# Kernel optimization log

Measured on AMD Instinct MI355X. Metric: run time of the kernel, lower is better.

The kernel has to match this reference:

```python
import jax, jax.numpy as jnp
import numpy as np

DIM = 1024
DEPTH = 8
DIM_HEAD = 64
HEADS = 16
NUM_Q = 16
EMB = 768
OUT = 1024
FF_INNER = 4 * DIM
INNER = DIM_HEAD * HEADS  # 1024
B, N1 = 64, 577
EPS = 1e-5


def _ln(x, g, b):
    mu = jnp.mean(x, axis=-1, keepdims=True)
    var = jnp.mean((x - mu) ** 2, axis=-1, keepdims=True)
    return (x - mu) * jax.lax.rsqrt(var + EPS) * g + b


def setup_inputs() -> dict:
    key = jax.random.key(0)
    ks = jax.random.split(key, 16)
    std = 0.02
    inp = {
        'x': jax.random.normal(ks[0], (B, N1, EMB), jnp.float32),
        'queries': jax.random.normal(ks[1], (1, NUM_Q, DIM), jnp.float32) / DIM ** 0.5,
        'proj_in_w': jax.random.normal(ks[2], (EMB, DIM), jnp.float32) * std,
        'proj_in_b': jnp.zeros((DIM,), jnp.float32),
        'ln1_g': jnp.ones((DEPTH, DIM), jnp.float32),
        'ln1_b': jnp.zeros((DEPTH, DIM), jnp.float32),
        'ln2_g': jnp.ones((DEPTH, DIM), jnp.float32),
        'ln2_b': jnp.zeros((DEPTH, DIM), jnp.float32),
        'wq': jax.random.normal(ks[3], (DEPTH, DIM, INNER), jnp.float32) * std,
        'wkv': jax.random.normal(ks[4], (DEPTH, DIM, 2 * INNER), jnp.float32) * std,
        'wo': jax.random.normal(ks[5], (DEPTH, INNER, DIM), jnp.float32) * std,
        'ffln_g': jnp.ones((DEPTH, DIM), jnp.float32),
        'ffln_b': jnp.zeros((DEPTH, DIM), jnp.float32),
        'w1': jax.random.normal(ks[6], (DEPTH, DIM, FF_INNER), jnp.float32) * std,
        'w2': jax.random.normal(ks[7], (DEPTH, FF_INNER, DIM), jnp.float32) * std,
        'proj_out_w': jax.random.normal(ks[8], (DIM, OUT), jnp.float32) * std,
        'proj_out_b': jnp.zeros((OUT,), jnp.float32),
        'nout_g': jnp.ones((OUT,), jnp.float32),
        'nout_b': jnp.zeros((OUT,), jnp.float32),
    }
    return inp


def reference(x, queries, proj_in_w, proj_in_b, ln1_g, ln1_b, ln2_g, ln2_b,
              wq, wkv, wo, ffln_g, ffln_b, w1, w2,
              proj_out_w, proj_out_b, nout_g, nout_b):
    b = x.shape[0]
    xp = x @ proj_in_w + proj_in_b          # (b, n1, dim)
    latents0 = jnp.broadcast_to(queries, (b, NUM_Q, DIM))
    scale = DIM_HEAD ** -0.25               # applied to both q and k

    def layer(latents, p):
        (g1, b1, g2, b2, Wq, Wkv, Wo, gf, bf, W1, W2) = p
        xn = _ln(xp, g1, b1)                # (b, n1, dim)
        lt = _ln(latents, g2, b2)           # (b, nq, dim)
        q = lt @ Wq                         # (b, nq, inner)
        kv_in = jnp.concatenate([xn, lt], axis=1)   # (b, n1+nq, dim)
        kv = kv_in @ Wkv                    # (b, n1+nq, 2*inner)
        k, v = jnp.split(kv, 2, axis=-1)
        L = kv_in.shape[1]
        qh = q.reshape(b, NUM_Q, HEADS, DIM_HEAD).transpose(0, 2, 1, 3)
        kh = k.reshape(b, L, HEADS, DIM_HEAD).transpose(0, 2, 1, 3)
        vh = v.reshape(b, L, HEADS, DIM_HEAD).transpose(0, 2, 1, 3)
        logits = jnp.einsum('bhqd,bhkd->bhqk', qh * scale, kh * scale)
        w = jax.nn.softmax(logits.astype(jnp.float32), axis=-1).astype(logits.dtype)
        o = jnp.einsum('bhqk,bhkd->bhqd', w, vh)
        o = o.transpose(0, 2, 1, 3).reshape(b, NUM_Q, INNER) @ Wo
        latents = o + latents
        h = _ln(latents, gf, bf) @ W1
        h = jax.nn.gelu(h, approximate=False)
        latents = h @ W2 + latents
        return latents, None

    params = (ln1_g, ln1_b, ln2_g, ln2_b, wq, wkv, wo, ffln_g, ffln_b, w1, w2)
    latents, _ = jax.lax.scan(layer, latents0, params)
    out = latents @ proj_out_w + proj_out_b
    return _ln(out, nout_g, nout_b)
```

## Files before the change

### kernel.cpp

```cpp
#include <hip/hip_runtime.h>
#include <hip/hip_bf16.h>
#include <math.h>

#define DEV __device__ __forceinline__

typedef __bf16 bf16x8 __attribute__((ext_vector_type(8)));
typedef float f32x4 __attribute__((ext_vector_type(4)));
typedef unsigned short u16x8 __attribute__((ext_vector_type(8)));
typedef unsigned short u16x4 __attribute__((ext_vector_type(4)));

DEV float b2f(unsigned short u){ unsigned int i = ((unsigned int)u)<<16; float f; __builtin_memcpy(&f,&i,4); return f; }
DEV unsigned short f2b(float x){ unsigned int i; __builtin_memcpy(&i,&x,4); unsigned int r = i + 0x7FFFu + ((i>>16)&1u); return (unsigned short)(r>>16); }

DEV int swz(int row, int elem){ return row*64 + ((((elem>>3) ^ row) & 7)<<3) + (elem&7); }

DEV int xcd_swz(int orig, int nwg){
  int q = nwg >> 3, r = nwg & 7;
  int x = orig & 7, idx = orig >> 3;
  return (x < r ? x*(q+1) : r*(q+1) + (x-r)*q) + idx;
}

enum { EPI_F32=0, EPI_GELU=2, EPI_RESF32=3 };

__global__ __launch_bounds__(512)
void gemm3(const unsigned short* __restrict__ A, const unsigned short* __restrict__ Bt,
           const float* __restrict__ bias, unsigned short* __restrict__ Out,
           int M, int N, int K, int NT)
{
    __shared__ unsigned short As[256*64];
    __shared__ unsigned short Bs[256*64];
    const int tid  = threadIdx.x;
    const int lane = tid & 63;
    const int wave = tid >> 6;
    const int wr = wave >> 2, wc = wave & 3;
    const int nb = xcd_swz(blockIdx.x, gridDim.x);
    const int nt = nb % NT, mt = nb / NT;

    f32x4 acc[8][4];
    #pragma unroll
    for (int m=0;m<8;m++)
      #pragma unroll
      for (int n=0;n<4;n++) acc[m][n] = f32x4{0.f,0.f,0.f,0.f};

    const unsigned short* pA[4]; const unsigned short* pB[4];
    int dA[4], dB[4];
    #pragma unroll
    for (int i=0;i<4;i++){
      int e = (i*512+tid)*8; int row = e>>6, col = e&63;
      int gr = mt*256 + row; if (gr > M-1) gr = M-1;
      pA[i] = A + (size_t)gr*K + col;
      dA[i] = swz(row,col);
      pB[i] = Bt + (size_t)(nt*256+row)*K + col;
      dB[i] = swz(row,col);
    }

    u16x8 rA[4], rB[4];
    auto issue = [&](int k0){
      #pragma unroll
      for (int i=0;i<4;i++) rA[i] = *reinterpret_cast<const u16x8*>(pA[i]+k0);
      #pragma unroll
      for (int i=0;i<4;i++) rB[i] = *reinterpret_cast<const u16x8*>(pB[i]+k0);
    };
    auto commit = [&](){
      #pragma unroll
      for (int i=0;i<4;i++) *reinterpret_cast<u16x8*>(&As[dA[i]]) = rA[i];
      #pragma unroll
      for (int i=0;i<4;i++) *reinterpret_cast<u16x8*>(&Bs[dB[i]]) = rB[i];
    };

    issue(0);
    const int nk = K / 64;
    #pragma unroll 1
    for (int kt=0; kt<nk; kt++){
      __syncthreads();
      commit();
      __syncthreads();
      if (kt+1 < nk) issue((kt+1)*64);
      #pragma unroll
      for (int kk=0; kk<2; kk++){
        bf16x8 bv[4];
        #pragma unroll
        for (int n=0;n<4;n++){
          int r = wc*64 + n*16 + (lane&15);
          bv[n] = (bf16x8)(*reinterpret_cast<const u16x8*>(&Bs[swz(r, kk*32 + (lane>>4)*8)]));
        }
        #pragma unroll
        for (int m=0;m<8;m++){
          int r = wr*128 + m*16 + (lane&15);
          bf16x8 av = (bf16x8)(*reinterpret_cast<const u16x8*>(&As[swz(r, kk*32 + (lane>>4)*8)]));
          #pragma unroll
          for (int n=0;n<4;n++)
            acc[m][n] = __builtin_amdgcn_mfma_f32_16x16x32_bf16(av, bv[n], acc[m][n], 0, 0, 0);
        }
      }
    }

    #pragma unroll
    for (int m=0;m<8;m++){
      #pragma unroll
      for (int n=0;n<4;n++){
        #pragma unroll
        for (int r=0;r<4;r++){
          int row = mt*256 + wr*128 + m*16 + (lane>>4)*4 + r;
          int col = nt*256 + wc*64 + n*16 + (lane&15);
          if (row < M){
            float v = acc[m][n][r];
            if (bias) v += bias[col];
            Out[(size_t)row*N + col] = f2b(v);
          }
        }
      }
    }
}

template<int EPI>
__global__ __launch_bounds__(256)
void gemm_sp2(const unsigned short* __restrict__ AH, const unsigned short* __restrict__ AL,
              const unsigned short* __restrict__ BH, const unsigned short* __restrict__ BL,
              const float* __restrict__ bias, const float* __restrict__ Res,
              void* __restrict__ Out, unsigned short* __restrict__ OutL,
              int M, int N, int K, int NT)
{
    constexpr int MR=2, NR=2;
    __shared__ unsigned short As[2*64*64];
    __shared__ unsigned short Bs[2*64*64];
    const int tid  = threadIdx.x;
    const int lane = tid & 63;
    const int wave = tid >> 6;
    const int wr = wave >> 1, wc = wave & 1;
    const int chunk = gridDim.x >> 3;
    const int nb = (blockIdx.x & 7)*chunk + (blockIdx.x >> 3);
    const int nt = nb % NT, mt = nb / NT;

    f32x4 acc[MR][NR];
    #pragma unroll
    for (int m=0;m<MR;m++)
      #pragma unroll
      for (int n=0;n<NR;n++) acc[m][n] = f32x4{0.f,0.f,0.f,0.f};

    const unsigned short *pA[2], *pB[2];
    int dst[2];
    #pragma unroll
    for (int i=0;i<2;i++){
      int e = (i*256+tid)*8; int row = e>>6, col = e&63;
      pA[i] = AH + (size_t)(mt*64+row)*K + col;
      pB[i] = BH + (size_t)(nt*64+row)*K + col;
      dst[i] = swz(row,col);
    }
    const size_t dAL = (size_t)(AL - AH);
    const size_t dBL = (size_t)(BL - BH);

    u16x8 rAH0[2], rAL0[2], rBH0[2], rBL0[2];
    u16x8 rAH1[2], rAL1[2], rBH1[2], rBL1[2];
    auto issue0 = [&](int k0){
      #pragma unroll
      for (int i=0;i<2;i++){
        rAH0[i] = *reinterpret_cast<const u16x8*>(pA[i]+k0);
        rAL0[i] = *reinterpret_cast<const u16x8*>(pA[i]+dAL+k0);
        rBH0[i] = *reinterpret_cast<const u16x8*>(pB[i]+k0);
        rBL0[i] = *reinterpret_cast<const u16x8*>(pB[i]+dBL+k0);
      }
    };
    auto issue1 = [&](int k0){
      #pragma unroll
      for (int i=0;i<2;i++){
        rAH1[i] = *reinterpret_cast<const u16x8*>(pA[i]+k0);
        rAL1[i] = *reinterpret_cast<const u16x8*>(pA[i]+dAL+k0);
        rBH1[i] = *reinterpret_cast<const u16x8*>(pB[i]+k0);
        rBL1[i] = *reinterpret_cast<const u16x8*>(pB[i]+dBL+k0);
      }
    };
    auto commit0 = [&](){
      #pragma unroll
      for (int i=0;i<2;i++){
        *reinterpret_cast<u16x8*>(&As[dst[i]])      = rAH0[i];
        *reinterpret_cast<u16x8*>(&As[4096+dst[i]]) = rAL0[i];
        *reinterpret_cast<u16x8*>(&Bs[dst[i]])      = rBH0[i];
        *reinterpret_cast<u16x8*>(&Bs[4096+dst[i]]) = rBL0[i];
      }
    };
    auto commit1 = [&](){
      #pragma unroll
      for (int i=0;i<2;i++){
        *reinterpret_cast<u16x8*>(&As[dst[i]])      = rAH1[i];
        *reinterpret_cast<u16x8*>(&As[4096+dst[i]]) = rAL1[i];
        *reinterpret_cast<u16x8*>(&Bs[dst[i]])      = rBH1[i];
        *reinterpret_cast<u16x8*>(&Bs[4096+dst[i]]) = rBL1[i];
      }
    };
    auto compute = [&](){
      #pragma unroll
      for (int kk=0; kk<2; kk++){
        bf16x8 ah[MR], al[MR], bh[NR], bl[NR];
        #pragma unroll
        for (int m=0;m<MR;m++){
          int a = swz(wr*32 + m*16 + (lane&15), kk*32 + (lane>>4)*8);
          ah[m] = (bf16x8)(*reinterpret_cast<const u16x8*>(&As[a]));
          al[m] = (bf16x8)(*reinterpret_cast<const u16x8*>(&As[4096 + a]));
        }
        #pragma unroll
        for (int n=0;n<NR;n++){
          int a = swz(wc*32 + n*16 + (lane&15), kk*32 + (lane>>4)*8);
          bh[n] = (bf16x8)(*reinterpret_cast<const u16x8*>(&Bs[a]));
          bl[n] = (bf16x8)(*reinterpret_cast<const u16x8*>(&Bs[4096 + a]));
        }
        #pragma unroll
        for (int m=0;m<MR;m++)
          #pragma unroll
          for (int n=0;n<NR;n++){
            acc[m][n] = __builtin_amdgcn_mfma_f32_16x16x32_bf16(ah[m], bh[n], acc[m][n], 0, 0, 0);
            acc[m][n] = __builtin_amdgcn_mfma_f32_16x16x32_bf16(ah[m], bl[n], acc[m][n], 0, 0, 0);
            acc[m][n] = __builtin_amdgcn_mfma_f32_16x16x32_bf16(al[m], bh[n], acc[m][n], 0, 0, 0);
          }
      }
    };

    const int nk = K / 64;
    issue0(0); issue1(64);
    #pragma unroll 1
    for (int kt=0; kt<nk; kt+=2){
      __syncthreads();
      commit0();
      __syncthreads();
      if (kt+2 < nk) issue0((kt+2)*64);
      compute();
      __syncthreads();
      commit1();
      __syncthreads();
      if (kt+3 < nk) issue1((kt+3)*64);
      compute();
    }

    #pragma unroll
    for (int m=0;m<MR;m++){
      #pragma unroll
      for (int n=0;n<NR;n++){
        #pragma unroll
        for (int r=0;r<4;r++){
          int row = mt*64 + wr*32 + m*16 + (lane>>4)*4 + r;
          int col = nt*64 + wc*32 + n*16 + (lane&15);
          float v = acc[m][n][r];
          if (bias) v += bias[col];
          if constexpr (EPI==EPI_GELU){
            v = 0.5f*v*(1.0f + erff(v*0.70710678118654752f));
            unsigned short hi = f2b(v);
            ((unsigned short*)Out)[(size_t)row*N + col] = hi;
            OutL[(size_t)row*N + col] = f2b(v - b2f(hi));
          } else {
            if constexpr (EPI==EPI_RESF32) v += Res[(size_t)row*N + col];
            ((float*)Out)[(size_t)row*N + col] = v;
          }
        }
      }
    }
}

enum { OM_F32=0, OM_BF16=1, OM_SPLIT=2 };
template<bool INF32, int OM, bool HASGB>
__global__ __launch_bounds__(256)
void ln_rows(const void* __restrict__ In, void* __restrict__ Out,
             unsigned short* __restrict__ OutL,
             const float* __restrict__ g, const float* __restrict__ bb)
{
  const int row = blockIdx.x;
  const int tid = threadIdx.x;
  const size_t base = (size_t)row*1024 + tid*4;
  float v[4];
  if constexpr (INF32){
    f32x4 t = *reinterpret_cast<const f32x4*>((const float*)In + base);
    v[0]=t[0]; v[1]=t[1]; v[2]=t[2]; v[3]=t[3];
  } else {
    u16x4 t = *reinterpret_cast<const u16x4*>((const unsigned short*)In + base);
    #pragma unroll
    for (int j=0;j<4;j++) v[j] = b2f(t[j]);
  }
  float s = v[0]+v[1]+v[2]+v[3];
  float q = v[0]*v[0]+v[1]*v[1]+v[2]*v[2]+v[3]*v[3];
  #pragma unroll
  for (int o=32;o>0;o>>=1){ s += __shfl_xor(s,o,64); q += __shfl_xor(q,o,64); }
  __shared__ float sm[8];
  const int wave = tid>>6, lane = tid&63;
  if (lane==0){ sm[wave] = s; sm[4+wave] = q; }
  __syncthreads();
  s = sm[0]+sm[1]+sm[2]+sm[3];
  q = sm[4]+sm[5]+sm[6]+sm[7];
  const float mean = s*(1.f/1024.f);
  const float rstd = rsqrtf(fmaxf(q*(1.f/1024.f) - mean*mean, 0.f) + 1e-5f);
  #pragma unroll
  for (int j=0;j<4;j++){
    float t2 = (v[j]-mean)*rstd;
    if constexpr (HASGB) t2 = t2*g[tid*4+j] + bb[tid*4+j];
    v[j] = t2;
  }
  if constexpr (OM==OM_F32){
    f32x4 t{v[0],v[1],v[2],v[3]};
    *reinterpret_cast<f32x4*>((float*)Out + base) = t;
  } else if constexpr (OM==OM_BF16){
    u16x4 t{f2b(v[0]),f2b(v[1]),f2b(v[2]),f2b(v[3])};
    *reinterpret_cast<u16x4*>((unsigned short*)Out + base) = t;
  } else {
    u16x4 h{f2b(v[0]),f2b(v[1]),f2b(v[2]),f2b(v[3])};
    u16x4 l{f2b(v[0]-b2f(h[0])),f2b(v[1]-b2f(h[1])),f2b(v[2]-b2f(h[2])),f2b(v[3]-b2f(h[3]))};
    *reinterpret_cast<u16x4*>((unsigned short*)Out + base) = h;
    *reinterpret_cast<u16x4*>(OutL + base) = l;
  }
}

template<bool LO>
__global__ __launch_bounds__(256)
void transpose_cvt_b(const float* __restrict__ W, const float* __restrict__ rs,
                     unsigned short* __restrict__ Wt, unsigned short* __restrict__ Wtlo,
                     int K, int N, size_t wLS, size_t tLS, int dstRowOff)
{
  const int l = blockIdx.z;
  const float* Wl = W + (size_t)l*wLS;
  __shared__ float t[32][33];
  const int tx = threadIdx.x & 31, ty = threadIdx.x >> 5;
  const int n0 = blockIdx.x*32, k0 = blockIdx.y*32;
  #pragma unroll
  for (int j=0;j<4;j++){
    int r = ty + j*8;
    float w = Wl[(size_t)(k0+r)*N + n0 + tx];
    if (rs) w *= rs[l*1024 + k0+r];
    t[r][tx] = w;
  }
  __syncthreads();
  #pragma unroll
  for (int j=0;j<4;j++){
    int r = ty + j*8;
    float w = t[tx][r];
    unsigned short hi = f2b(w);
    size_t di = (size_t)l*tLS + (size_t)(dstRowOff + n0 + r)*K + k0 + tx;
    Wt[di] = hi;
    if constexpr (LO) Wtlo[di] = f2b(w - b2f(hi));
  }
}

__global__ __launch_bounds__(256)
void biaskv_kernel(const float* __restrict__ ln1b, const float* __restrict__ wkv,
                   float* __restrict__ out)
{
  const int l = blockIdx.y;
  const int n = blockIdx.x*256 + threadIdx.x;
  const float* b1 = ln1b + l*1024;
  const float* W  = wkv + (size_t)l*1024*2048;
  float s = 0.f;
  for (int k=0;k<1024;k++) s += b1[k]*W[(size_t)k*2048 + n];
  out[l*2048 + n] = s;
}

__global__ __launch_bounds__(256)
void init_latents(const float* __restrict__ Q, float* __restrict__ L)
{
  size_t idx = ((size_t)blockIdx.x*256 + threadIdx.x)*4;
  int row = (int)(idx >> 10);
  int col = (int)(idx & 1023);
  f32x4 t = *reinterpret_cast<const f32x4*>(Q + (size_t)(row & 15)*1024 + col);
  *reinterpret_cast<f32x4*>(L + idx) = t;
}

__global__ __launch_bounds__(256)
void cvt_f32_bf16(const float* __restrict__ In, unsigned short* __restrict__ Out, size_t n4)
{
  size_t i = (size_t)blockIdx.x*256 + threadIdx.x;
  if (i >= n4) return;
  f32x4 t = *reinterpret_cast<const f32x4*>(In + i*4);
  u16x4 u{f2b(t[0]),f2b(t[1]),f2b(t[2]),f2b(t[3])};
  *reinterpret_cast<u16x4*>(Out + i*4) = u;
}

__global__ __launch_bounds__(256)
void cvt_f32b_pair(const float* __restrict__ In, unsigned short* __restrict__ Oh,
                   unsigned short* __restrict__ Ol)
{
  size_t idx = ((size_t)blockIdx.x*256 + threadIdx.x)*4;
  f32x4 t = *reinterpret_cast<const f32x4*>(In + idx);
  u16x4 h{f2b(t[0]),f2b(t[1]),f2b(t[2]),f2b(t[3])};
  u16x4 l{f2b(t[0]-b2f(h[0])),f2b(t[1]-b2f(h[1])),f2b(t[2]-b2f(h[2])),f2b(t[3]-b2f(h[3]))};
  *reinterpret_cast<u16x4*>(Oh + idx) = h;
  *reinterpret_cast<u16x4*>(Ol + idx) = l;
}

__global__ __launch_bounds__(256)
void attn_kernel(const float* __restrict__ QKVf,
                 const unsigned short* __restrict__ KVX,
                 unsigned short* __restrict__ ATTOh,
                 unsigned short* __restrict__ ATTOl)
{
  __shared__ float qs[16][64];
  __shared__ float ws[16][600];
  const int tid = threadIdx.x;
  const int bh = blockIdx.x;
  const int b = bh >> 4, h = bh & 15;

  {
    int idx = tid*4;
    int qi = idx >> 6, d = idx & 63;
    f32x4 t = *reinterpret_cast<const f32x4*>(QKVf + (size_t)(b*16+qi)*3072 + h*64 + d);
    #pragma unroll
    for (int j=0;j<4;j++) qs[qi][d+j] = 0.125f * t[j];
  }
  __syncthreads();

  for (int r = tid; r < 593; r += 256){
    float a[16];
    #pragma unroll
    for (int qi=0;qi<16;qi++) a[qi] = 0.f;
    if (r < 577){
      const unsigned short* krow = KVX + ((size_t)(b*577 + r)*2048 + h*64);
      #pragma unroll 4
      for (int d4=0; d4<16; d4++){
        u16x4 k4 = *reinterpret_cast<const u16x4*>(krow + d4*4);
        float kf0=b2f(k4[0]), kf1=b2f(k4[1]), kf2=b2f(k4[2]), kf3=b2f(k4[3]);
        #pragma unroll
        for (int qi=0;qi<16;qi++){
          f32x4 q4 = *reinterpret_cast<const f32x4*>(&qs[qi][d4*4]);
          a[qi] += q4[0]*kf0 + q4[1]*kf1 + q4[2]*kf2 + q4[3]*kf3;
        }
      }
    } else {
      const float* krow = QKVf + (size_t)(b*16 + (r-577))*3072 + 1024 + h*64;
      #pragma unroll 4
      for (int d4=0; d4<16; d4++){
        f32x4 k4 = *reinterpret_cast<const f32x4*>(krow + d4*4);
        #pragma unroll
        for (int qi=0;qi<16;qi++){
          f32x4 q4 = *reinterpret_cast<const f32x4*>(&qs[qi][d4*4]);
          a[qi] += q4[0]*k4[0] + q4[1]*k4[1] + q4[2]*k4[2] + q4[3]*k4[3];
        }
      }
    }
    #pragma unroll
    for (int qi=0;qi<16;qi++) ws[qi][r] = a[qi];
  }
  __syncthreads();

  const int wave = tid>>6, lane = tid&63;
  for (int qi = wave; qi < 16; qi += 4){
    float m = -1e30f;
    for (int r = lane; r < 593; r += 64) m = fmaxf(m, ws[qi][r]);
    #pragma unroll
    for (int o=32;o>0;o>>=1) m = fmaxf(m, __shfl_xor(m,o,64));
    float s = 0.f;
    for (int r = lane; r < 593; r += 64){ float e = expf(ws[qi][r]-m); ws[qi][r] = e; s += e; }
    #pragma unroll
    for (int o=32;o>0;o>>=1) s += __shfl_xor(s,o,64);
    float inv = 1.f/s;
    for (int r = lane; r < 593; r += 64) ws[qi][r] *= inv;
  }
  __syncthreads();

  const int d = tid & 63, qg = tid >> 6;
  float o0=0.f,o1=0.f,o2=0.f,o3=0.f;
  for (int rr=0; rr<576; rr+=4){
    f32x4 w0 = *reinterpret_cast<const f32x4*>(&ws[qg   ][rr]);
    f32x4 w1 = *reinterpret_cast<const f32x4*>(&ws[qg+4 ][rr]);
    f32x4 w2 = *reinterpret_cast<const f32x4*>(&ws[qg+8 ][rr]);
    f32x4 w3 = *reinterpret_cast<const f32x4*>(&ws[qg+12][rr]);
    #pragma unroll
    for (int j=0;j<4;j++){
      const unsigned short* vrow = KVX + ((size_t)(b*577 + rr + j)*2048 + 1024 + h*64);
      float v = b2f(vrow[d]);
      o0 += w0[j]*v; o1 += w1[j]*v; o2 += w2[j]*v; o3 += w3[j]*v;
    }
  }
  {
    float v = b2f(KVX[(size_t)(b*577 + 576)*2048 + 1024 + h*64 + d]);
    o0 += ws[qg][576]*v; o1 += ws[qg+4][576]*v; o2 += ws[qg+8][576]*v; o3 += ws[qg+12][576]*v;
  }
  for (int r=577; r<593; r++){
    float v = QKVf[(size_t)(b*16 + (r-577))*3072 + 2048 + h*64 + d];
    o0 += ws[qg][r]*v; o1 += ws[qg+4][r]*v; o2 += ws[qg+8][r]*v; o3 += ws[qg+12][r]*v;
  }
  float ov[4] = {o0,o1,o2,o3};
  #pragma unroll
  for (int j=0;j<4;j++){
    size_t idx = (size_t)(b*16+qg+4*j)*1024 + h*64 + d;
    unsigned short hi = f2b(ov[j]);
    ATTOh[idx] = hi;
    ATTOl[idx] = f2b(ov[j] - b2f(hi));
  }
}

extern "C" void kernel_launch(void* const* d_in, const int* in_sizes, int n_in,
                              void* d_out, int out_size, void* d_ws, size_t ws_size,
                              hipStream_t stream)
{
  const float* x    = (const float*)d_in[0];
  const float* qry  = (const float*)d_in[1];
  const float* piw  = (const float*)d_in[2];
  const float* pib  = (const float*)d_in[3];
  const float* ln1g = (const float*)d_in[4];
  const float* ln1b = (const float*)d_in[5];
  const float* ln2g = (const float*)d_in[6];
  const float* ln2b = (const float*)d_in[7];
  const float* wq   = (const float*)d_in[8];
  const float* wkv  = (const float*)d_in[9];
  const float* wo   = (const float*)d_in[10];
  const float* ffg  = (const float*)d_in[11];
  const float* ffb  = (const float*)d_in[12];
  const float* w1   = (const float*)d_in[13];
  const float* w2   = (const float*)d_in[14];
  const float* pow_ = (const float*)d_in[15];
  const float* pob  = (const float*)d_in[16];
  const float* ng   = (const float*)d_in[17];
  const float* nb   = (const float*)d_in[18];

  const int MROWS = 64*577;
  char* wsb = (char*)d_ws;
  size_t off = 0;
  auto alloc = [&](size_t bytes)->char*{
    char* p = wsb + off; off = (off + bytes + 255) & ~(size_t)255; return p;
  };
  unsigned short* XB     = (unsigned short*)alloc((size_t)36992*768*2);
  unsigned short* XP     = (unsigned short*)alloc((size_t)36992*1024*2);
  unsigned short* KVX    = (unsigned short*)alloc((size_t)36992*2048*2);
  unsigned short* WpiT   = (unsigned short*)alloc((size_t)1024*768*2);
  unsigned short* WkvTs  = (unsigned short*)alloc((size_t)8*2048*1024*2);
  unsigned short* WqkvT  = (unsigned short*)alloc((size_t)8*3072*1024*2);
  unsigned short* WqkvTl = (unsigned short*)alloc((size_t)8*3072*1024*2);
  unsigned short* WoT    = (unsigned short*)alloc((size_t)8*1024*1024*2);
  unsigned short* WoTl   = (unsigned short*)alloc((size_t)8*1024*1024*2);
  unsigned short* W1T    = (unsigned short*)alloc((size_t)4096*1024*2);
  unsigned short* W1Tl   = (unsigned short*)alloc((size_t)4096*1024*2);
  unsigned short* W2T    = (unsigned short*)alloc((size_t)1024*4096*2);
  unsigned short* W2Tl   = (unsigned short*)alloc((size_t)1024*4096*2);
  float*          BKV    = (float*)alloc((size_t)8*2048*4);
  unsigned short* LTh    = (unsigned short*)alloc((size_t)1024*1024*2);
  unsigned short* LTl    = (unsigned short*)alloc((size_t)1024*1024*2);
  float*          QKVf   = (float*)alloc((size_t)1024*3072*4);
  unsigned short* ATTOh  = (unsigned short*)alloc((size_t)1024*1024*2);
  unsigned short* ATTOl  = (unsigned short*)alloc((size_t)1024*1024*2);
  unsigned short* FFHh   = (unsigned short*)alloc((size_t)1024*4096*2);
  unsigned short* FFHl   = (unsigned short*)alloc((size_t)1024*4096*2);
  unsigned short* LATBh  = (unsigned short*)alloc((size_t)1024*1024*2);
  unsigned short* LATBl  = (unsigned short*)alloc((size_t)1024*1024*2);
  float*          LATF   = (float*)alloc((size_t)1024*1024*4);
  if (off > ws_size) return;

  dim3 blk(256);
  dim3 blk5(512);

  cvt_f32_bf16<<<dim3((36928*768/4 + 255)/256), blk, 0, stream>>>(x, XB, (size_t)36928*768/4);
  transpose_cvt_b<false><<<dim3(32,24,1), blk, 0, stream>>>(piw, nullptr, WpiT, nullptr, 768, 1024, 0, 0, 0);
  transpose_cvt_b<false><<<dim3(64,32,8), blk, 0, stream>>>(wkv, ln1g, WkvTs, nullptr, 1024, 2048, (size_t)1024*2048, (size_t)2048*1024, 0);
  transpose_cvt_b<true ><<<dim3(32,32,8), blk, 0, stream>>>(wq,  nullptr, WqkvT, WqkvTl, 1024, 1024, (size_t)1024*1024, (size_t)3072*1024, 0);
  transpose_cvt_b<true ><<<dim3(64,32,8), blk, 0, stream>>>(wkv, nullptr, WqkvT, WqkvTl, 1024, 2048, (size_t)1024*2048, (size_t)3072*1024, 1024);
  transpose_cvt_b<true ><<<dim3(32,32,8), blk, 0, stream>>>(wo,  nullptr, WoT, WoTl, 1024, 1024, (size_t)1024*1024, (size_t)1024*1024, 0);
  biaskv_kernel<<<dim3(8,8), blk, 0, stream>>>(ln1b, wkv, BKV);
  init_latents<<<dim3(1024), blk, 0, stream>>>(qry, LATF);

  gemm3<<<dim3(145*4), blk5, 0, stream>>>(XB, WpiT, pib, XP, MROWS, 1024, 768, 4);
  ln_rows<false,OM_BF16,false><<<dim3(MROWS), blk, 0, stream>>>(XP, XP, nullptr, nullptr, nullptr);

  for (int l=0; l<8; l++){
    transpose_cvt_b<true><<<dim3(128,32,1), blk, 0, stream>>>(w1 + (size_t)l*1024*4096, nullptr, W1T, W1Tl, 1024, 4096, 0, 0, 0);
    transpose_cvt_b<true><<<dim3(32,128,1), blk, 0, stream>>>(w2 + (size_t)l*4096*1024, nullptr, W2T, W2Tl, 4096, 1024, 0, 0, 0);

    ln_rows<true,OM_SPLIT,true><<<dim3(1024), blk, 0, stream>>>(LATF, LTh, LTl, ln2g + l*1024, ln2b + l*1024);
    gemm_sp2<EPI_F32><<<dim3(16*48), blk, 0, stream>>>(
        LTh, LTl, WqkvT + (size_t)l*3072*1024, WqkvTl + (size_t)l*3072*1024,
        nullptr, nullptr, QKVf, nullptr, 1024, 3072, 1024, 48);
    gemm3<<<dim3(145*8), blk5, 0, stream>>>(
        XP, WkvTs + (size_t)l*2048*1024, BKV + l*2048, KVX, MROWS, 2048, 1024, 8);
    attn_kernel<<<dim3(1024), blk, 0, stream>>>(QKVf, KVX, ATTOh, ATTOl);
    gemm_sp2<EPI_RESF32><<<dim3(16*16), blk, 0, stream>>>(
        ATTOh, ATTOl, WoT + (size_t)l*1024*1024, WoTl + (size_t)l*1024*1024,
        nullptr, LATF, LATF, nullptr, 1024, 1024, 1024, 16);
    ln_rows<true,OM_SPLIT,true><<<dim3(1024), blk, 0, stream>>>(LATF, LTh, LTl, ffg + l*1024, ffb + l*1024);
    gemm_sp2<EPI_GELU><<<dim3(16*64), blk, 0, stream>>>(
        LTh, LTl, W1T, W1Tl, nullptr, nullptr, FFHh, FFHl, 1024, 4096, 1024, 64);
    gemm_sp2<EPI_RESF32><<<dim3(16*16), blk, 0, stream>>>(
        FFHh, FFHl, W2T, W2Tl, nullptr, LATF, LATF, nullptr, 1024, 1024, 4096, 16);
  }

  transpose_cvt_b<true><<<dim3(32,32,1), blk, 0, stream>>>(pow_, nullptr, W1T, W1Tl, 1024, 1024, 0, 0, 0);
  cvt_f32b_pair<<<dim3(1024), blk, 0, stream>>>(LATF, LATBh, LATBl);
  gemm_sp2<EPI_F32><<<dim3(16*16), blk, 0, stream>>>(
      LATBh, LATBl, W1T, W1Tl, pob, nullptr, QKVf, nullptr, 1024, 1024, 1024, 16);
  ln_rows<true,OM_F32,true><<<dim3(1024), blk, 0, stream>>>(QKVf, d_out, nullptr, ng, nb);
}
```

Before: 5.023 ms.

## Split-K the FF2 GEMM into four chunks with residual reduce, add sched barriers

```diff
diff --git a/kernel.cpp b/kernel.cpp
--- a/kernel.cpp
+++ b/kernel.cpp
@@ -76,6 +76,7 @@
       commit();
       __syncthreads();
       if (kt+1 < nk) issue((kt+1)*64);
+      __builtin_amdgcn_sched_barrier(0);
       #pragma unroll
       for (int kk=0; kk<2; kk++){
         bf16x8 bv[4];
@@ -223,11 +224,13 @@
       commit0();
       __syncthreads();
       if (kt+2 < nk) issue0((kt+2)*64);
+      __builtin_amdgcn_sched_barrier(0);
       compute();
       __syncthreads();
       commit1();
       __syncthreads();
       if (kt+3 < nk) issue1((kt+3)*64);
+      __builtin_amdgcn_sched_barrier(0);
       compute();
     }
 
@@ -253,6 +256,156 @@
         }
       }
     }
+}
+
+__global__ __launch_bounds__(256)
+void gemm_spk(const unsigned short* __restrict__ AH, const unsigned short* __restrict__ AL,
+              const unsigned short* __restrict__ BH, const unsigned short* __restrict__ BL,
+              float* __restrict__ PART, int M, int N, int Kstride, int Klen, int NT)
+{
+    constexpr int MR=2, NR=2;
+    __shared__ unsigned short As[2*64*64];
+    __shared__ unsigned short Bs[2*64*64];
+    const int tid  = threadIdx.x;
+    const int lane = tid & 63;
+    const int wave = tid >> 6;
+    const int wr = wave >> 1, wc = wave & 1;
+    const int nblk = (M>>6)*(N>>6);
+    const int kchunk = blockIdx.x / nblk;
+    const int rem = blockIdx.x - kchunk*nblk;
+    const int cpx = nblk >> 3;
+    const int nb = (rem & 7)*cpx + (rem >> 3);
+    const int nt = nb % NT, mt = nb / NT;
+    const int kbase = kchunk*Klen;
+
+    f32x4 acc[MR][NR];
+    #pragma unroll
+    for (int m=0;m<MR;m++)
+      #pragma unroll
+      for (int n=0;n<NR;n++) acc[m][n] = f32x4{0.f,0.f,0.f,0.f};
+
+    const unsigned short *pA[2], *pB[2];
+    int dst[2];
+    #pragma unroll
+    for (int i=0;i<2;i++){
+      int e = (i*256+tid)*8; int row = e>>6, col = e&63;
+      pA[i] = AH + (size_t)(mt*64+row)*Kstride + kbase + col;
+      pB[i] = BH + (size_t)(nt*64+row)*Kstride + kbase + col;
+      dst[i] = swz(row,col);
+    }
+    const size_t dAL = (size_t)(AL - AH);
+    const size_t dBL = (size_t)(BL - BH);
+
+    u16x8 rAH0[2], rAL0[2], rBH0[2], rBL0[2];
+    u16x8 rAH1[2], rAL1[2], rBH1[2], rBL1[2];
+    auto issue0 = [&](int k0){
+      #pragma unroll
+      for (int i=0;i<2;i++){
+        rAH0[i] = *reinterpret_cast<const u16x8*>(pA[i]+k0);
+        rAL0[i] = *reinterpret_cast<const u16x8*>(pA[i]+dAL+k0);
+        rBH0[i] = *reinterpret_cast<const u16x8*>(pB[i]+k0);
+        rBL0[i] = *reinterpret_cast<const u16x8*>(pB[i]+dBL+k0);
+      }
+    };
+    auto issue1 = [&](int k0){
+      #pragma unroll
+      for (int i=0;i<2;i++){
+        rAH1[i] = *reinterpret_cast<const u16x8*>(pA[i]+k0);
+        rAL1[i] = *reinterpret_cast<const u16x8*>(pA[i]+dAL+k0);
+        rBH1[i] = *reinterpret_cast<const u16x8*>(pB[i]+k0);
+        rBL1[i] = *reinterpret_cast<const u16x8*>(pB[i]+dBL+k0);
+      }
+    };
+    auto commit0 = [&](){
+      #pragma unroll
+      for (int i=0;i<2;i++){
+        *reinterpret_cast<u16x8*>(&As[dst[i]])      = rAH0[i];
+        *reinterpret_cast<u16x8*>(&As[4096+dst[i]]) = rAL0[i];
+        *reinterpret_cast<u16x8*>(&Bs[dst[i]])      = rBH0[i];
+        *reinterpret_cast<u16x8*>(&Bs[4096+dst[i]]) = rBL0[i];
+      }
+    };
+    auto commit1 = [&](){
+      #pragma unroll
+      for (int i=0;i<2;i++){
+        *reinterpret_cast<u16x8*>(&As[dst[i]])      = rAH1[i];
+        *reinterpret_cast<u16x8*>(&As[4096+dst[i]]) = rAL1[i];
+        *reinterpret_cast<u16x8*>(&Bs[dst[i]])      = rBH1[i];
+        *reinterpret_cast<u16x8*>(&Bs[4096+dst[i]]) = rBL1[i];
+      }
+    };
+    auto compute = [&](){
+      #pragma unroll
+      for (int kk=0; kk<2; kk++){
+        bf16x8 ah[MR], al[MR], bh[NR], bl[NR];
+        #pragma unroll
+        for (int m=0;m<MR;m++){
+          int a = swz(wr*32 + m*16 + (lane&15), kk*32 + (lane>>4)*8);
+          ah[m] = (bf16x8)(*reinterpret_cast<const u16x8*>(&As[a]));
+          al[m] = (bf16x8)(*reinterpret_cast<const u16x8*>(&As[4096 + a]));
+        }
+        #pragma unroll
+        for (int n=0;n<NR;n++){
+          int a = swz(wc*32 + n*16 + (lane&15), kk*32 + (lane>>4)*8);
+          bh[n] = (bf16x8)(*reinterpret_cast<const u16x8*>(&Bs[a]));
+          bl[n] = (bf16x8)(*reinterpret_cast<const u16x8*>(&Bs[4096 + a]));
+        }
+        #pragma unroll
+        for (int m=0;m<MR;m++)
+          #pragma unroll
+          for (int n=0;n<NR;n++){
+            acc[m][n] = __builtin_amdgcn_mfma_f32_16x16x32_bf16(ah[m], bh[n], acc[m][n], 0, 0, 0);
+            acc[m][n] = __builtin_amdgcn_mfma_f32_16x16x32_bf16(ah[m], bl[n], acc[m][n], 0, 0, 0);
+            acc[m][n] = __builtin_amdgcn_mfma_f32_16x16x32_bf16(al[m], bh[n], acc[m][n], 0, 0, 0);
+          }
+      }
+    };
+
+    const int nk = Klen / 64;
+    issue0(0); issue1(64);
+    #pragma unroll 1
+    for (int kt=0; kt<nk; kt+=2){
+      __syncthreads();
+      commit0();
+      __syncthreads();
+      if (kt+2 < nk) issue0((kt+2)*64);
+      __builtin_amdgcn_sched_barrier(0);
+      compute();
+      __syncthreads();
+      commit1();
+      __syncthreads();
+      if (kt+3 < nk) issue1((kt+3)*64);
+      __builtin_amdgcn_sched_barrier(0);
+      compute();
+    }
+
+    float* out = PART + (size_t)kchunk*M*N;
+    #pragma unroll
+    for (int m=0;m<MR;m++){
+      #pragma unroll
+      for (int n=0;n<NR;n++){
+        #pragma unroll
+        for (int r=0;r<4;r++){
+          int row = mt*64 + wr*32 + m*16 + (lane>>4)*4 + r;
+          int col = nt*64 + wc*32 + n*16 + (lane&15);
+          out[(size_t)row*N + col] = acc[m][n][r];
+        }
+      }
+    }
+}
+
+__global__ __launch_bounds__(256)
+void reduce4_res(const float* __restrict__ PART, float* __restrict__ LATF)
+{
+  size_t i = ((size_t)blockIdx.x*256 + threadIdx.x)*4;
+  f32x4 a = *reinterpret_cast<const f32x4*>(PART + i);
+  f32x4 b = *reinterpret_cast<const f32x4*>(PART + 1048576 + i);
+  f32x4 c = *reinterpret_cast<const f32x4*>(PART + 2097152 + i);
+  f32x4 d = *reinterpret_cast<const f32x4*>(PART + 3145728 + i);
+  f32x4 r = *reinterpret_cast<f32x4*>(LATF + i);
+  #pragma unroll
+  for (int j=0;j<4;j++) r[j] += a[j]+b[j]+c[j]+d[j];
+  *reinterpret_cast<f32x4*>(LATF + i) = r;
 }
 
 enum { OM_F32=0, OM_BF16=1, OM_SPLIT=2 };
@@ -537,6 +690,7 @@
   unsigned short* LATBl  = (unsigned short*)alloc((size_t)1024*1024*2);
   float*          LATF   = (float*)alloc((size_t)1024*1024*4);
   if (off > ws_size) return;
+  float* PART = (float*)XB;
 
   dim3 blk(256);
   dim3 blk5(512);
@@ -570,8 +724,9 @@
     ln_rows<true,OM_SPLIT,true><<<dim3(1024), blk, 0, stream>>>(LATF, LTh, LTl, ffg + l*1024, ffb + l*1024);
     gemm_sp2<EPI_GELU><<<dim3(16*64), blk, 0, stream>>>(
         LTh, LTl, W1T, W1Tl, nullptr, nullptr, FFHh, FFHl, 1024, 4096, 1024, 64);
-    gemm_sp2<EPI_RESF32><<<dim3(16*16), blk, 0, stream>>>(
-        FFHh, FFHl, W2T, W2Tl, nullptr, LATF, LATF, nullptr, 1024, 1024, 4096, 16);
+    gemm_spk<<<dim3(4*16*16), blk, 0, stream>>>(
+        FFHh, FFHl, W2T, W2Tl, PART, 1024, 1024, 4096, 1024, 16);
+    reduce4_res<<<dim3(1024), blk, 0, stream>>>(PART, LATF);
   }
 
   transpose_cvt_b<true><<<dim3(32,32,1), blk, 0, stream>>>(pow_, nullptr, W1T, W1Tl, 1024, 1024, 0, 0, 0);
```

Result: no change. 4.956 ms (-1.3%).
